# Kernel optimization log

Hardware: AMD Instinct MI355X
Metric: run time of the kernel (lower is better)

## Reference

```python
import jax, jax.numpy as jnp
import numpy as np

N, E = 10000, 320000
IN_CH, HID, HEADS, OUT_CH = 128, 64, 4, 64
NEG_SLOPE = 0.2


def gat_conv(x, edge_index, edge_attr, W, a_src, a_dst, a_edge, W_edge, bias,
             heads, out_ch, concat):
    """PyG-style GATConv with edge_dim features.
    x: [N, F_in], edge_index: [2, E] (row0=src, row1=dst), edge_attr: [E, edge_dim].
    W: [F_in, heads*out_ch], a_*: [heads, out_ch], W_edge: [edge_dim, heads*out_ch],
    bias: [heads*out_ch] if concat else [out_ch].
    """
    n = x.shape[0]
    xh = (x @ W).reshape(n, heads, out_ch)                       # [N,H,C]
    src, dst = edge_index[0], edge_index[1]
    al_s = jnp.einsum('nhc,hc->nh', xh, a_src)                   # [N,H]
    al_d = jnp.einsum('nhc,hc->nh', xh, a_dst)                   # [N,H]
    eh = (edge_attr @ W_edge).reshape(-1, heads, out_ch)         # [E,H,C]
    al_e = jnp.einsum('ehc,hc->eh', eh, a_edge)                  # [E,H]
    alpha = jax.nn.leaky_relu(al_s[src] + al_d[dst] + al_e, NEG_SLOPE)  # [E,H]
    # segment softmax over incoming edges of each destination node
    amax = jax.ops.segment_max(alpha, dst, num_segments=n)       # [N,H]
    amax = jax.lax.stop_gradient(jnp.where(jnp.isfinite(amax), amax, 0.0))
    ex = jnp.exp(alpha - amax[dst])
    denom = jax.ops.segment_sum(ex, dst, num_segments=n)         # [N,H]
    att = ex / (denom[dst] + 1e-16)                              # [E,H]
    out = jax.ops.segment_sum(xh[src] * att[:, :, None], dst, num_segments=n)  # [N,H,C]
    out = out.reshape(n, heads * out_ch) if concat else out.mean(axis=1)
    return out + bias


def setup_inputs() -> dict:
    key = jax.random.key(0)
    ks = jax.random.split(key, 16)
    s1 = 1.0 / np.sqrt(IN_CH)
    s2 = 1.0 / np.sqrt(HEADS * HID)
    return {
        'x': jax.random.normal(ks[0], (N, IN_CH), dtype=jnp.float32),
        'edge_weight': jax.random.uniform(ks[1], (E, 1), dtype=jnp.float32),
        'W1': jax.random.normal(ks[2], (IN_CH, HEADS * HID), dtype=jnp.float32) * s1,
        'a_src1': jax.random.normal(ks[3], (HEADS, HID), dtype=jnp.float32) * s2,
        'a_dst1': jax.random.normal(ks[4], (HEADS, HID), dtype=jnp.float32) * s2,
        'a_edge1': jax.random.normal(ks[5], (HEADS, HID), dtype=jnp.float32) * s2,
        'We1': jax.random.normal(ks[6], (1, HEADS * HID), dtype=jnp.float32),
        'b1': jnp.zeros((HEADS * HID,), dtype=jnp.float32),
        'W2': jax.random.normal(ks[7], (HEADS * HID, OUT_CH), dtype=jnp.float32) * s2,
        'a_src2': jax.random.normal(ks[8], (1, OUT_CH), dtype=jnp.float32) * s2,
        'a_dst2': jax.random.normal(ks[9], (1, OUT_CH), dtype=jnp.float32) * s2,
        'a_edge2': jax.random.normal(ks[10], (1, OUT_CH), dtype=jnp.float32) * s2,
        'We2': jax.random.normal(ks[11], (1, OUT_CH), dtype=jnp.float32),
        'b2': jnp.zeros((OUT_CH,), dtype=jnp.float32),
        'edge_index': jax.random.randint(ks[12], (2, E), 0, N, dtype=jnp.int64
                                         if jax.config.jax_enable_x64 else jnp.int32),
    }


def reference(x, edge_weight, W1, a_src1, a_dst1, a_edge1, We1, b1,
              W2, a_src2, a_dst2, a_edge2, We2, b2, edge_index):
    h = gat_conv(x, edge_index, edge_weight, W1, a_src1, a_dst1, a_edge1, We1, b1,
                 heads=HEADS, out_ch=HID, concat=True)
    h = jax.nn.elu(h)
    out = gat_conv(h, edge_index, edge_weight, W2, a_src2, a_dst2, a_edge2, We2, b2,
                   heads=1, out_ch=OUT_CH, concat=False)
    return out
```

## Files before the change

### kernel.cpp

```cpp
#include <hip/hip_runtime.h>

constexpr int N_NODES = 10000;
constexpr int N_EDGES = 320000;
constexpr int IN_CH   = 128;
constexpr int HID     = 64;
constexpr int HEADS   = 4;
constexpr int OUT_CH  = 64;
constexpr int F1      = HEADS * HID;
constexpr int CAP     = 128;
constexpr float NEG_SLOPE = 0.2f;
constexpr int GEMM_BLOCKS = (N_NODES + 31) / 32;
constexpr int EDGE_BLOCKS = N_EDGES / 256;


__global__ void k_init(int* __restrict__ cnt,
                       const float* __restrict__ We1, const float* __restrict__ ae1,
                       const float* __restrict__ We2, const float* __restrict__ ae2,
                       float* __restrict__ de) {
    int bid = blockIdx.x;
    if (bid < 40) {
        int i = bid * 256 + threadIdx.x;
        if (i < N_NODES) cnt[i] = 0;
        return;
    }
    int t = threadIdx.x;
    if (t < HEADS) {
        float s = 0.f;
        for (int c = 0; c < HID; ++c) s = fmaf(We1[t * HID + c], ae1[t * HID + c], s);
        de[t] = s;
    } else if (t == HEADS) {
        float s = 0.f;
        for (int c = 0; c < OUT_CH; ++c) s = fmaf(We2[c], ae2[c], s);
        de[HEADS] = s;
    }
}


__global__ __launch_bounds__(256) void k_gemm1(const float* __restrict__ x,
                                               const float* __restrict__ W,
                                               const float* __restrict__ a_src,
                                               const float* __restrict__ a_dst,
                                               float* __restrict__ xh1T,
                                               float* __restrict__ als4,
                                               float* __restrict__ ald4) {
    __shared__ float xs[32 * IN_CH];
    int tid = threadIdx.x;
    int row0 = blockIdx.x * 32;
    int nrows = N_NODES - row0; if (nrows > 32) nrows = 32;
    float4* xs4 = (float4*)xs;
    const float4* xg = (const float4*)(x + (size_t)row0 * IN_CH);
    #pragma unroll
    for (int j = 0; j < 4; ++j) {
        int idx = tid + j * 256;
        if ((idx >> 5) < nrows) xs4[idx] = xg[idx];
    }
    __syncthreads();
    int wv = tid >> 6;
    int lane = tid & 63;
    int col = lane * 4;
    int h = lane >> 4;
    int c = (lane & 15) * 4;
    float acc[8][4];
    #pragma unroll
    for (int m = 0; m < 8; ++m)
        #pragma unroll
        for (int j = 0; j < 4; ++j) acc[m][j] = 0.f;

    for (int k = 0; k < IN_CH; k += 4) {
        float4 w0 = *(const float4*)(W + (size_t)(k + 0) * F1 + col);
        float4 w1 = *(const float4*)(W + (size_t)(k + 1) * F1 + col);
        float4 w2 = *(const float4*)(W + (size_t)(k + 2) * F1 + col);
        float4 w3 = *(const float4*)(W + (size_t)(k + 3) * F1 + col);
        #pragma unroll
        for (int m = 0; m < 8; ++m) {
            float4 xv = *(const float4*)(xs + (wv * 8 + m) * IN_CH + k);
            acc[m][0] = fmaf(xv.x, w0.x, fmaf(xv.y, w1.x, fmaf(xv.z, w2.x, fmaf(xv.w, w3.x, acc[m][0]))));
            acc[m][1] = fmaf(xv.x, w0.y, fmaf(xv.y, w1.y, fmaf(xv.z, w2.y, fmaf(xv.w, w3.y, acc[m][1]))));
            acc[m][2] = fmaf(xv.x, w0.z, fmaf(xv.y, w1.z, fmaf(xv.z, w2.z, fmaf(xv.w, w3.z, acc[m][2]))));
            acc[m][3] = fmaf(xv.x, w0.w, fmaf(xv.y, w1.w, fmaf(xv.z, w2.w, fmaf(xv.w, w3.w, acc[m][3]))));
        }
    }
    float4 asv = *(const float4*)(a_src + h * HID + c);
    float4 adv = *(const float4*)(a_dst + h * HID + c);
    #pragma unroll
    for (int m = 0; m < 8; ++m) {
        int row = wv * 8 + m;
        if (row < nrows)
            *(float4*)(xh1T + ((size_t)h * N_NODES + row0 + row) * HID + c) = *(float4*)acc[m];
        float s = acc[m][0] * asv.x + acc[m][1] * asv.y + acc[m][2] * asv.z + acc[m][3] * asv.w;
        float d = acc[m][0] * adv.x + acc[m][1] * adv.y + acc[m][2] * adv.z + acc[m][3] * adv.w;
        #pragma unroll
        for (int off = 1; off < 16; off <<= 1) {
            s += __shfl_xor(s, off, 64);
            d += __shfl_xor(d, off, 64);
        }
        if ((lane & 15) == 0 && row < nrows) {
            als4[(size_t)(row0 + row) * HEADS + h] = s;
            ald4[(size_t)(row0 + row) * HEADS + h] = d;
        }
    }
}


__global__ void k_fill(const int* __restrict__ src, const int* __restrict__ dst,
                       const float* __restrict__ ew,
                       const float* __restrict__ als4, const float* __restrict__ ald4,
                       const float* __restrict__ de, int* __restrict__ cnt,
                       int* __restrict__ srcs_pad, float* __restrict__ ewc_pad,
                       float* __restrict__ ex_pad) {
    int e = blockIdx.x * 256 + threadIdx.x;
    int s = src[e], d = dst[e];
    float w = ew[e];
    int pos = atomicAdd(&cnt[d], 1);
    if (pos >= CAP) return;
    srcs_pad[(size_t)d * CAP + pos] = s;
    ewc_pad[(size_t)d * CAP + pos] = w;
    float4 as = *(const float4*)(als4 + (size_t)s * HEADS);
    float4 ad = *(const float4*)(ald4 + (size_t)d * HEADS);
    float4 dv = *(const float4*)de;
    float4 a;
    a.x = as.x + ad.x + w * dv.x;
    a.y = as.y + ad.y + w * dv.y;
    a.z = as.z + ad.z + w * dv.z;
    a.w = as.w + ad.w + w * dv.w;
    a.x = a.x > 0.f ? a.x : NEG_SLOPE * a.x;
    a.y = a.y > 0.f ? a.y : NEG_SLOPE * a.y;
    a.z = a.z > 0.f ? a.z : NEG_SLOPE * a.z;
    a.w = a.w > 0.f ? a.w : NEG_SLOPE * a.w;
    size_t eb = (size_t)d * HEADS * CAP + pos;
    ex_pad[eb + 0 * CAP] = __expf(a.x);
    ex_pad[eb + 1 * CAP] = __expf(a.y);
    ex_pad[eb + 2 * CAP] = __expf(a.z);
    ex_pad[eb + 3 * CAP] = __expf(a.w);
}


__global__ __launch_bounds__(256) void k_agg1(
        const float* __restrict__ xh1T, const float* __restrict__ ex_pad,
        const int* __restrict__ srcs_pad, const int* __restrict__ cnt,
        const float* __restrict__ bias, float* __restrict__ h1) {
    int b = blockIdx.x;
    int slot8 = b & 7;
    int h = slot8 >> 1;
    int nb = (b >> 3) * 2 + (slot8 & 1);
    int node = nb * 4 + (threadIdx.x >> 6);
    int lane = threadIdx.x & 63;
    int es = lane >> 4;
    int c4 = (lane & 15) * 4;
    const float* xb  = xh1T + (size_t)h * N_NODES * HID;
    const float* exb = ex_pad + ((size_t)node * HEADS + h) * CAP;
    const int*   sp  = srcs_pad + (size_t)node * CAP;
    int n = cnt[node]; if (n > CAP) n = CAP;
    float4 acc = make_float4(0.f, 0.f, 0.f, 0.f);
    float den = 0.f;
    int i = es;
    for (; i + 4 < n; i += 8) {
        float e0 = exb[i], e1 = exb[i + 4];
        int s0 = sp[i], s1 = sp[i + 4];
        float4 x0 = *(const float4*)(xb + (size_t)s0 * HID + c4);
        float4 x1 = *(const float4*)(xb + (size_t)s1 * HID + c4);
        den += e0 + e1;
        acc.x = fmaf(e0, x0.x, fmaf(e1, x1.x, acc.x));
        acc.y = fmaf(e0, x0.y, fmaf(e1, x1.y, acc.y));
        acc.z = fmaf(e0, x0.z, fmaf(e1, x1.z, acc.z));
        acc.w = fmaf(e0, x0.w, fmaf(e1, x1.w, acc.w));
    }
    if (i < n) {
        float e0 = exb[i];
        int s0 = sp[i];
        float4 x0 = *(const float4*)(xb + (size_t)s0 * HID + c4);
        den += e0;
        acc.x = fmaf(e0, x0.x, acc.x);
        acc.y = fmaf(e0, x0.y, acc.y);
        acc.z = fmaf(e0, x0.z, acc.z);
        acc.w = fmaf(e0, x0.w, acc.w);
    }
    #pragma unroll
    for (int off = 32; off >= 16; off >>= 1) {
        acc.x += __shfl_xor(acc.x, off, 64);
        acc.y += __shfl_xor(acc.y, off, 64);
        acc.z += __shfl_xor(acc.z, off, 64);
        acc.w += __shfl_xor(acc.w, off, 64);
        den   += __shfl_xor(den,   off, 64);
    }
    if (es == 0) {
        float inv = 1.f / (den + 1e-16f);
        int cb = h * HID + c4;
        float4 o;
        o.x = fmaf(acc.x, inv, bias[cb + 0]);
        o.y = fmaf(acc.y, inv, bias[cb + 1]);
        o.z = fmaf(acc.z, inv, bias[cb + 2]);
        o.w = fmaf(acc.w, inv, bias[cb + 3]);
        o.x = o.x > 0.f ? o.x : expm1f(o.x);
        o.y = o.y > 0.f ? o.y : expm1f(o.y);
        o.z = o.z > 0.f ? o.z : expm1f(o.z);
        o.w = o.w > 0.f ? o.w : expm1f(o.w);
        *(float4*)(h1 + (size_t)node * F1 + cb) = o;
    }
}


__global__ __launch_bounds__(256) void k_gemm2(const float* __restrict__ hin,
                                               const float* __restrict__ W,
                                               const float* __restrict__ a_src,
                                               const float* __restrict__ a_dst,
                                               float* __restrict__ xh2,
                                               float* __restrict__ als,
                                               float* __restrict__ ald) {
    __shared__ float hs[32 * F1];
    int tid = threadIdx.x;
    int row0 = blockIdx.x * 32;
    int nrows = N_NODES - row0; if (nrows > 32) nrows = 32;
    float4* hs4 = (float4*)hs;
    const float4* hg = (const float4*)(hin + (size_t)row0 * F1);
    #pragma unroll
    for (int j = 0; j < 8; ++j) {
        int idx = tid + j * 256;
        if ((idx >> 6) < nrows) hs4[idx] = hg[idx];
    }
    __syncthreads();
    int rowg = tid >> 4;
    int col = (tid & 15) * 4;
    float acc[2][4];
    #pragma unroll
    for (int m = 0; m < 2; ++m)
        #pragma unroll
        for (int j = 0; j < 4; ++j) acc[m][j] = 0.f;
    for (int k = 0; k < F1; k += 4) {
        float4 w0 = *(const float4*)(W + (size_t)(k + 0) * OUT_CH + col);
        float4 w1 = *(const float4*)(W + (size_t)(k + 1) * OUT_CH + col);
        float4 w2 = *(const float4*)(W + (size_t)(k + 2) * OUT_CH + col);
        float4 w3 = *(const float4*)(W + (size_t)(k + 3) * OUT_CH + col);
        #pragma unroll
        for (int m = 0; m < 2; ++m) {
            float4 xv = *(const float4*)(hs + (rowg * 2 + m) * F1 + k);
            acc[m][0] = fmaf(xv.x, w0.x, fmaf(xv.y, w1.x, fmaf(xv.z, w2.x, fmaf(xv.w, w3.x, acc[m][0]))));
            acc[m][1] = fmaf(xv.x, w0.y, fmaf(xv.y, w1.y, fmaf(xv.z, w2.y, fmaf(xv.w, w3.y, acc[m][1]))));
            acc[m][2] = fmaf(xv.x, w0.z, fmaf(xv.y, w1.z, fmaf(xv.z, w2.z, fmaf(xv.w, w3.z, acc[m][2]))));
            acc[m][3] = fmaf(xv.x, w0.w, fmaf(xv.y, w1.w, fmaf(xv.z, w2.w, fmaf(xv.w, w3.w, acc[m][3]))));
        }
    }
    int lane = tid & 63;
    float4 asv = *(const float4*)(a_src + col);
    float4 adv = *(const float4*)(a_dst + col);
    #pragma unroll
    for (int m = 0; m < 2; ++m) {
        int row = rowg * 2 + m;
        if (row < nrows) *(float4*)(xh2 + (size_t)(row0 + row) * OUT_CH + col) = *(float4*)acc[m];
        float s = acc[m][0] * asv.x + acc[m][1] * asv.y + acc[m][2] * asv.z + acc[m][3] * asv.w;
        float d = acc[m][0] * adv.x + acc[m][1] * adv.y + acc[m][2] * adv.z + acc[m][3] * adv.w;
        #pragma unroll
        for (int off = 1; off < 16; off <<= 1) {
            s += __shfl_xor(s, off, 64);
            d += __shfl_xor(d, off, 64);
        }
        if ((lane & 15) == 0 && row < nrows) {
            als[row0 + row] = s;
            ald[row0 + row] = d;
        }
    }
}


__global__ __launch_bounds__(256) void k_agg2(
        const float* __restrict__ xh2, const float* __restrict__ als,
        const float* __restrict__ ald, const float* __restrict__ ewc_pad,
        const int* __restrict__ srcs_pad, const int* __restrict__ cnt,
        const float* __restrict__ de, const float* __restrict__ bias,
        float* __restrict__ out) {
    int node = blockIdx.x * 4 + (threadIdx.x >> 6);
    int lane = threadIdx.x & 63;
    int es = lane >> 4;
    int c4 = (lane & 15) * 4;
    float de2  = de[HEADS];
    float aldv = ald[node];
    const int*   sp = srcs_pad + (size_t)node * CAP;
    const float* wp = ewc_pad + (size_t)node * CAP;
    int n = cnt[node]; if (n > CAP) n = CAP;
    float4 acc = make_float4(0.f, 0.f, 0.f, 0.f);
    float den = 0.f;
    int i = es;
    for (; i + 4 < n; i += 8) {
        int s0 = sp[i], s1 = sp[i + 4];
        float w0 = wp[i], w1 = wp[i + 4];
        float a0 = als[s0] + aldv + w0 * de2;
        float a1 = als[s1] + aldv + w1 * de2;
        a0 = a0 > 0.f ? a0 : NEG_SLOPE * a0;
        a1 = a1 > 0.f ? a1 : NEG_SLOPE * a1;
        float e0 = __expf(a0), e1 = __expf(a1);
        float4 x0 = *(const float4*)(xh2 + (size_t)s0 * OUT_CH + c4);
        float4 x1 = *(const float4*)(xh2 + (size_t)s1 * OUT_CH + c4);
        den += e0 + e1;
        acc.x = fmaf(e0, x0.x, fmaf(e1, x1.x, acc.x));
        acc.y = fmaf(e0, x0.y, fmaf(e1, x1.y, acc.y));
        acc.z = fmaf(e0, x0.z, fmaf(e1, x1.z, acc.z));
        acc.w = fmaf(e0, x0.w, fmaf(e1, x1.w, acc.w));
    }
    if (i < n) {
        int s0 = sp[i];
        float w0 = wp[i];
        float a0 = als[s0] + aldv + w0 * de2;
        a0 = a0 > 0.f ? a0 : NEG_SLOPE * a0;
        float e0 = __expf(a0);
        float4 x0 = *(const float4*)(xh2 + (size_t)s0 * OUT_CH + c4);
        den += e0;
        acc.x = fmaf(e0, x0.x, acc.x);
        acc.y = fmaf(e0, x0.y, acc.y);
        acc.z = fmaf(e0, x0.z, acc.z);
        acc.w = fmaf(e0, x0.w, acc.w);
    }
    #pragma unroll
    for (int off = 32; off >= 16; off >>= 1) {
        acc.x += __shfl_xor(acc.x, off, 64);
        acc.y += __shfl_xor(acc.y, off, 64);
        acc.z += __shfl_xor(acc.z, off, 64);
        acc.w += __shfl_xor(acc.w, off, 64);
        den   += __shfl_xor(den,   off, 64);
    }
    if (es == 0) {
        float inv = 1.f / (den + 1e-16f);
        float4 o;
        o.x = fmaf(acc.x, inv, bias[c4 + 0]);
        o.y = fmaf(acc.y, inv, bias[c4 + 1]);
        o.z = fmaf(acc.z, inv, bias[c4 + 2]);
        o.w = fmaf(acc.w, inv, bias[c4 + 3]);
        *(float4*)(out + (size_t)node * OUT_CH + c4) = o;
    }
}


extern "C" void kernel_launch(void* const* d_in, const int* in_sizes, int n_in,
                              void* d_out, int out_size, void* d_ws, size_t ws_size,
                              hipStream_t stream) {
    const float* x       = (const float*)d_in[0];
    const float* ew      = (const float*)d_in[1];
    const float* W1      = (const float*)d_in[2];
    const float* a_src1  = (const float*)d_in[3];
    const float* a_dst1  = (const float*)d_in[4];
    const float* a_edge1 = (const float*)d_in[5];
    const float* We1     = (const float*)d_in[6];
    const float* b1      = (const float*)d_in[7];
    const float* W2      = (const float*)d_in[8];
    const float* a_src2  = (const float*)d_in[9];
    const float* a_dst2  = (const float*)d_in[10];
    const float* a_edge2 = (const float*)d_in[11];
    const float* We2     = (const float*)d_in[12];
    const float* b2      = (const float*)d_in[13];
    const int*   eidx    = (const int*)d_in[14];
    const int* esrc = eidx;
    const int* edst = eidx + N_EDGES;
    float* out = (float*)d_out;

    char* p = (char*)d_ws;
    auto alloc = [&](size_t bytes) {
        char* r = p;
        p += (bytes + 255) & ~(size_t)255;
        return r;
    };
    float* xh1T     = (float*)alloc((size_t)N_NODES * F1 * 4);
    float* h1       = (float*)alloc((size_t)N_NODES * F1 * 4);
    float* xh2      = (float*)alloc((size_t)N_NODES * OUT_CH * 4);
    float* als4     = (float*)alloc((size_t)N_NODES * HEADS * 4);
    float* ald4     = (float*)alloc((size_t)N_NODES * HEADS * 4);
    float* als2     = (float*)alloc((size_t)N_NODES * 4);
    float* ald2     = (float*)alloc((size_t)N_NODES * 4);
    float* de       = (float*)alloc(8 * 4);
    int*   cnt      = (int*)alloc((size_t)N_NODES * 4);
    int*   srcs_pad = (int*)alloc((size_t)N_NODES * CAP * 4);
    float* ewc_pad  = (float*)alloc((size_t)N_NODES * CAP * 4);
    float* ex_pad   = (float*)alloc((size_t)N_NODES * HEADS * CAP * 4);

    k_init<<<41, 256, 0, stream>>>(cnt, We1, a_edge1, We2, a_edge2, de);

    k_gemm1<<<GEMM_BLOCKS, 256, 0, stream>>>(x, W1, a_src1, a_dst1, xh1T, als4, ald4);

    k_fill<<<EDGE_BLOCKS, 256, 0, stream>>>(esrc, edst, ew, als4, ald4, de,
                                            cnt, srcs_pad, ewc_pad, ex_pad);

    k_agg1<<<N_NODES / 4 * HEADS, 256, 0, stream>>>(xh1T, ex_pad, srcs_pad, cnt, b1, h1);

    k_gemm2<<<GEMM_BLOCKS, 256, 0, stream>>>(h1, W2, a_src2, a_dst2, xh2, als2, ald2);
    k_agg2<<<N_NODES / 4, 256, 0, stream>>>(xh2, als2, ald2, ewc_pad, srcs_pad, cnt,
                                            de, b2, out);
}
```

Baseline: 134.5 us.

## Pack edge src/weight and per-head exp into interleaved arrays; two edges per thread

Merges the padded source-index and edge-weight arrays into one int2 array and stores the four per-head exp values for each edge as a single float4, so the fill kernel issues one vector store per array instead of several scattered scalar stores. Each fill thread now handles two edges to overlap the atomics and gathers. The aggregation kernels read the packed layouts, which makes agg1's per-head exp reads strided by four floats instead of contiguous.

```diff
diff --git a/kernel.cpp b/kernel.cpp
--- a/kernel.cpp
+++ b/kernel.cpp
@@ -10,7 +10,7 @@
 constexpr int CAP     = 128;
 constexpr float NEG_SLOPE = 0.2f;
 constexpr int GEMM_BLOCKS = (N_NODES + 31) / 32;
-constexpr int EDGE_BLOCKS = N_EDGES / 256;
+constexpr int HALF_E = N_EDGES / 2;
 
 
 __global__ void k_init(int* __restrict__ cnt,
@@ -106,38 +106,55 @@
                        const float* __restrict__ ew,
                        const float* __restrict__ als4, const float* __restrict__ ald4,
                        const float* __restrict__ de, int* __restrict__ cnt,
-                       int* __restrict__ srcs_pad, float* __restrict__ ewc_pad,
-                       float* __restrict__ ex_pad) {
-    int e = blockIdx.x * 256 + threadIdx.x;
-    int s = src[e], d = dst[e];
-    float w = ew[e];
-    int pos = atomicAdd(&cnt[d], 1);
-    if (pos >= CAP) return;
-    srcs_pad[(size_t)d * CAP + pos] = s;
-    ewc_pad[(size_t)d * CAP + pos] = w;
-    float4 as = *(const float4*)(als4 + (size_t)s * HEADS);
-    float4 ad = *(const float4*)(ald4 + (size_t)d * HEADS);
+                       int2* __restrict__ sw_pad, float4* __restrict__ ex_pad4) {
+    int e0 = blockIdx.x * 256 + threadIdx.x;
+    int e1 = e0 + HALF_E;
+    int s0 = src[e0], d0 = dst[e0];
+    int s1 = src[e1], d1 = dst[e1];
+    float w0 = ew[e0], w1 = ew[e1];
+    int p0 = atomicAdd(&cnt[d0], 1);
+    int p1 = atomicAdd(&cnt[d1], 1);
+    float4 as0 = *(const float4*)(als4 + (size_t)s0 * HEADS);
+    float4 as1 = *(const float4*)(als4 + (size_t)s1 * HEADS);
+    float4 ad0 = *(const float4*)(ald4 + (size_t)d0 * HEADS);
+    float4 ad1 = *(const float4*)(ald4 + (size_t)d1 * HEADS);
     float4 dv = *(const float4*)de;
-    float4 a;
-    a.x = as.x + ad.x + w * dv.x;
-    a.y = as.y + ad.y + w * dv.y;
-    a.z = as.z + ad.z + w * dv.z;
-    a.w = as.w + ad.w + w * dv.w;
-    a.x = a.x > 0.f ? a.x : NEG_SLOPE * a.x;
-    a.y = a.y > 0.f ? a.y : NEG_SLOPE * a.y;
-    a.z = a.z > 0.f ? a.z : NEG_SLOPE * a.z;
-    a.w = a.w > 0.f ? a.w : NEG_SLOPE * a.w;
-    size_t eb = (size_t)d * HEADS * CAP + pos;
-    ex_pad[eb + 0 * CAP] = __expf(a.x);
-    ex_pad[eb + 1 * CAP] = __expf(a.y);
-    ex_pad[eb + 2 * CAP] = __expf(a.z);
-    ex_pad[eb + 3 * CAP] = __expf(a.w);
+    if (p0 < CAP) {
+        size_t q = (size_t)d0 * CAP + p0;
+        sw_pad[q] = make_int2(s0, __float_as_int(w0));
+        float4 a;
+        a.x = as0.x + ad0.x + w0 * dv.x;
+        a.y = as0.y + ad0.y + w0 * dv.y;
+        a.z = as0.z + ad0.z + w0 * dv.z;
+        a.w = as0.w + ad0.w + w0 * dv.w;
+        a.x = a.x > 0.f ? a.x : NEG_SLOPE * a.x;
+        a.y = a.y > 0.f ? a.y : NEG_SLOPE * a.y;
+        a.z = a.z > 0.f ? a.z : NEG_SLOPE * a.z;
+        a.w = a.w > 0.f ? a.w : NEG_SLOPE * a.w;
+        a.x = __expf(a.x); a.y = __expf(a.y); a.z = __expf(a.z); a.w = __expf(a.w);
+        ex_pad4[q] = a;
+    }
+    if (p1 < CAP) {
+        size_t q = (size_t)d1 * CAP + p1;
+        sw_pad[q] = make_int2(s1, __float_as_int(w1));
+        float4 a;
+        a.x = as1.x + ad1.x + w1 * dv.x;
+        a.y = as1.y + ad1.y + w1 * dv.y;
+        a.z = as1.z + ad1.z + w1 * dv.z;
+        a.w = as1.w + ad1.w + w1 * dv.w;
+        a.x = a.x > 0.f ? a.x : NEG_SLOPE * a.x;
+        a.y = a.y > 0.f ? a.y : NEG_SLOPE * a.y;
+        a.z = a.z > 0.f ? a.z : NEG_SLOPE * a.z;
+        a.w = a.w > 0.f ? a.w : NEG_SLOPE * a.w;
+        a.x = __expf(a.x); a.y = __expf(a.y); a.z = __expf(a.z); a.w = __expf(a.w);
+        ex_pad4[q] = a;
+    }
 }
 
 
 __global__ __launch_bounds__(256) void k_agg1(
-        const float* __restrict__ xh1T, const float* __restrict__ ex_pad,
-        const int* __restrict__ srcs_pad, const int* __restrict__ cnt,
+        const float* __restrict__ xh1T, const float4* __restrict__ ex_pad4,
+        const int2* __restrict__ sw_pad, const int* __restrict__ cnt,
         const float* __restrict__ bias, float* __restrict__ h1) {
     int b = blockIdx.x;
     int slot8 = b & 7;
@@ -148,15 +165,15 @@
     int es = lane >> 4;
     int c4 = (lane & 15) * 4;
     const float* xb  = xh1T + (size_t)h * N_NODES * HID;
-    const float* exb = ex_pad + ((size_t)node * HEADS + h) * CAP;
-    const int*   sp  = srcs_pad + (size_t)node * CAP;
+    const float* exb = (const float*)(ex_pad4 + (size_t)node * CAP) + h;
+    const int2*  sp  = sw_pad + (size_t)node * CAP;
     int n = cnt[node]; if (n > CAP) n = CAP;
     float4 acc = make_float4(0.f, 0.f, 0.f, 0.f);
     float den = 0.f;
     int i = es;
     for (; i + 4 < n; i += 8) {
-        float e0 = exb[i], e1 = exb[i + 4];
-        int s0 = sp[i], s1 = sp[i + 4];
+        float e0 = exb[i * 4], e1 = exb[(i + 4) * 4];
+        int s0 = sp[i].x, s1 = sp[i + 4].x;
         float4 x0 = *(const float4*)(xb + (size_t)s0 * HID + c4);
         float4 x1 = *(const float4*)(xb + (size_t)s1 * HID + c4);
         den += e0 + e1;
@@ -166,8 +183,8 @@
         acc.w = fmaf(e0, x0.w, fmaf(e1, x1.w, acc.w));
     }
     if (i < n) {
-        float e0 = exb[i];
-        int s0 = sp[i];
+        float e0 = exb[i * 4];
+        int s0 = sp[i].x;
         float4 x0 = *(const float4*)(xb + (size_t)s0 * HID + c4);
         den += e0;
         acc.x = fmaf(e0, x0.x, acc.x);
@@ -264,25 +281,24 @@
 
 __global__ __launch_bounds__(256) void k_agg2(
         const float* __restrict__ xh2, const float* __restrict__ als,
-        const float* __restrict__ ald, const float* __restrict__ ewc_pad,
-        const int* __restrict__ srcs_pad, const int* __restrict__ cnt,
-        const float* __restrict__ de, const float* __restrict__ bias,
-        float* __restrict__ out) {
+        const float* __restrict__ ald, const int2* __restrict__ sw_pad,
+        const int* __restrict__ cnt, const float* __restrict__ de,
+        const float* __restrict__ bias, float* __restrict__ out) {
     int node = blockIdx.x * 4 + (threadIdx.x >> 6);
     int lane = threadIdx.x & 63;
     int es = lane >> 4;
     int c4 = (lane & 15) * 4;
     float de2  = de[HEADS];
     float aldv = ald[node];
-    const int*   sp = srcs_pad + (size_t)node * CAP;
-    const float* wp = ewc_pad + (size_t)node * CAP;
+    const int2* sp = sw_pad + (size_t)node * CAP;
     int n = cnt[node]; if (n > CAP) n = CAP;
     float4 acc = make_float4(0.f, 0.f, 0.f, 0.f);
     float den = 0.f;
     int i = es;
     for (; i + 4 < n; i += 8) {
-        int s0 = sp[i], s1 = sp[i + 4];
-        float w0 = wp[i], w1 = wp[i + 4];
+        int2 sw0 = sp[i], sw1 = sp[i + 4];
+        int s0 = sw0.x, s1 = sw1.x;
+        float w0 = __int_as_float(sw0.y), w1 = __int_as_float(sw1.y);
         float a0 = als[s0] + aldv + w0 * de2;
         float a1 = als[s1] + aldv + w1 * de2;
         a0 = a0 > 0.f ? a0 : NEG_SLOPE * a0;
@@ -297,8 +313,9 @@
         acc.w = fmaf(e0, x0.w, fmaf(e1, x1.w, acc.w));
     }
     if (i < n) {
-        int s0 = sp[i];
-        float w0 = wp[i];
+        int2 sw0 = sp[i];
+        int s0 = sw0.x;
+        float w0 = __int_as_float(sw0.y);
         float a0 = als[s0] + aldv + w0 * de2;
         a0 = a0 > 0.f ? a0 : NEG_SLOPE * a0;
         float e0 = __expf(a0);
@@ -366,20 +383,18 @@
     float* ald2     = (float*)alloc((size_t)N_NODES * 4);
     float* de       = (float*)alloc(8 * 4);
     int*   cnt      = (int*)alloc((size_t)N_NODES * 4);
-    int*   srcs_pad = (int*)alloc((size_t)N_NODES * CAP * 4);
-    float* ewc_pad  = (float*)alloc((size_t)N_NODES * CAP * 4);
-    float* ex_pad   = (float*)alloc((size_t)N_NODES * HEADS * CAP * 4);
+    int2*  sw_pad   = (int2*)alloc((size_t)N_NODES * CAP * 8);
+    float4* ex_pad4 = (float4*)alloc((size_t)N_NODES * CAP * 16);
 
     k_init<<<41, 256, 0, stream>>>(cnt, We1, a_edge1, We2, a_edge2, de);
 
     k_gemm1<<<GEMM_BLOCKS, 256, 0, stream>>>(x, W1, a_src1, a_dst1, xh1T, als4, ald4);
 
-    k_fill<<<EDGE_BLOCKS, 256, 0, stream>>>(esrc, edst, ew, als4, ald4, de,
-                                            cnt, srcs_pad, ewc_pad, ex_pad);
-
-    k_agg1<<<N_NODES / 4 * HEADS, 256, 0, stream>>>(xh1T, ex_pad, srcs_pad, cnt, b1, h1);
+    k_fill<<<HALF_E / 256, 256, 0, stream>>>(esrc, edst, ew, als4, ald4, de,
+                                             cnt, sw_pad, ex_pad4);
+
+    k_agg1<<<N_NODES / 4 * HEADS, 256, 0, stream>>>(xh1T, ex_pad4, sw_pad, cnt, b1, h1);
 
     k_gemm2<<<GEMM_BLOCKS, 256, 0, stream>>>(h1, W2, a_src2, a_dst2, xh2, als2, ald2);
-    k_agg2<<<N_NODES / 4, 256, 0, stream>>>(xh2, als2, ald2, ewc_pad, srcs_pad, cnt,
-                                            de, b2, out);
-}
+    k_agg2<<<N_NODES / 4, 256, 0, stream>>>(xh2, als2, ald2, sw_pad, cnt, de, b2, out);
+}
```

After: 121.7 us. 1.11x faster.
